# Kernel optimization log

Measured on AMD Instinct MI355X. Metric: run time of the kernel, lower is better.

The kernel has to match this reference:

```python
import jax, jax.numpy as jnp
import numpy as np

NUM_IMGS = 8192
NUM_CAPS = 8192
R = 7        # views per image
D = 256      # embedding dim


def setup_inputs() -> dict:
    key = jax.random.key(0)
    k1, k2 = jax.random.split(key)
    imgs = jax.random.normal(k1, (NUM_IMGS, R, D), dtype=jnp.float32)
    caps = jax.random.normal(k2, (NUM_CAPS, D), dtype=jnp.float32)
    return {"imgs": imgs, "caps": caps}


def reference(imgs, caps):
    # scores[i, r, c] = <imgs[i, r], caps[c]>  then max over views r
    # matches torch.matmul(imgs, caps.t()).max(1)[0]
    scores = jnp.einsum("ird,cd->irc", imgs, caps)  # [num_imgs, r, num_caps]
    return scores.max(axis=1)                        # [num_imgs, num_caps]
```

## Files before the change

kernel.cpp:

```cpp
#include <hip/hip_runtime.h>
#include <hip/hip_bf16.h>
#include <cstdint>
#include <cstddef>

#define NI 8192
#define NC 8192
#define RV 7
#define DD 256

typedef __bf16  bf16x8 __attribute__((ext_vector_type(8)));
typedef float   f32x4  __attribute__((ext_vector_type(4)));
typedef __fp16  f16x2  __attribute__((ext_vector_type(2)));

#define IMGS_WS_BYTES (32u * 56u * 16384u)
#define CAPS_WS_OFF   IMGS_WS_BYTES
#define CAPS_WS_BYTES (64u * 65536u)
#define WS_NEEDED     ((size_t)(IMGS_WS_BYTES + CAPS_WS_BYTES))

static __device__ __forceinline__ unsigned pkbf(float x, float y) {
  unsigned a = __float_as_uint(x) + 0x8000u;
  unsigned b = __float_as_uint(y) + 0x8000u;
  return __builtin_amdgcn_perm(b, a, 0x07060302u);
}

static __device__ __forceinline__ void gload16(const void* g, void* l) {
  __builtin_amdgcn_global_load_lds(
      (const __attribute__((address_space(1))) void*)g,
      (__attribute__((address_space(3))) void*)l, 16, 0, 0);
}

__global__ __launch_bounds__(256)
void conv_imgs(const float* __restrict__ imgs, uint4* __restrict__ ws) {
  unsigned T = blockIdx.x * 256u + threadIdx.x;
  unsigned img = T / 224u;
  unsigned rem = T - img * 224u;
  unsigned r  = rem >> 5;
  unsigned ju = rem & 31u;
  const float* s = imgs + ((size_t)img * RV + r) * DD + ju * 8u;
  float4 a = *(const float4*)s;
  float4 b = *(const float4*)(s + 4);
  uint4 v = { pkbf(a.x, a.y), pkbf(a.z, a.w), pkbf(b.x, b.y), pkbf(b.z, b.w) };
  unsigned ib = img >> 8, lrow = img & 255u;
  unsigned j = ju >> 2, u = ju & 3u;
  unsigned t = r * 8u + j;
  unsigned byteoff = (ib * 56u + t) * 16384u + u * 4096u + lrow * 16u;
  ws[byteoff >> 4] = v;
}

__global__ __launch_bounds__(256)
void conv_caps(const float* __restrict__ caps, uint4* __restrict__ ws) {
  unsigned T = blockIdx.x * 256u + threadIdx.x;
  unsigned gr = T >> 5;
  unsigned ju = T & 31u;
  const float* s = caps + (size_t)gr * DD + ju * 8u;
  float4 a = *(const float4*)s;
  float4 b = *(const float4*)(s + 4);
  uint4 v = { pkbf(a.x, a.y), pkbf(a.z, a.w), pkbf(b.x, b.y), pkbf(b.z, b.w) };
  unsigned cb = gr >> 7, row = gr & 127u;
  unsigned j = ju >> 2, u = ju & 3u;
  unsigned byteoff = cb * 65536u + j * 8192u + u * 2048u + row * 16u;
  ws[byteoff >> 4] = v;
}

#define LOAD_SET(P, BUFN, JN)                                   \
  P##a0 = *(const bf16x8*)(aF + (BUFN)*16384 + 0*256);          \
  P##a1 = *(const bf16x8*)(aF + (BUFN)*16384 + 1*256);          \
  P##a2 = *(const bf16x8*)(aF + (BUFN)*16384 + 2*256);          \
  P##a3 = *(const bf16x8*)(aF + (BUFN)*16384 + 3*256);          \
  P##b0 = *(const bf16x8*)(bF + (JN)*8192 + 0*256);             \
  P##b1 = *(const bf16x8*)(bF + (JN)*8192 + 1*256);             \
  P##b2 = *(const bf16x8*)(bF + (JN)*8192 + 2*256);             \
  P##b3 = *(const bf16x8*)(bF + (JN)*8192 + 3*256);

#define MFMA_SET(P)                                                              \
  acc[0][0] = __builtin_amdgcn_mfma_f32_16x16x32_bf16(P##a0, P##b0, acc[0][0], 0, 0, 0); \
  acc[1][0] = __builtin_amdgcn_mfma_f32_16x16x32_bf16(P##a1, P##b0, acc[1][0], 0, 0, 0); \
  acc[2][0] = __builtin_amdgcn_mfma_f32_16x16x32_bf16(P##a2, P##b0, acc[2][0], 0, 0, 0); \
  acc[3][0] = __builtin_amdgcn_mfma_f32_16x16x32_bf16(P##a3, P##b0, acc[3][0], 0, 0, 0); \
  acc[0][1] = __builtin_amdgcn_mfma_f32_16x16x32_bf16(P##a0, P##b1, acc[0][1], 0, 0, 0); \
  acc[1][1] = __builtin_amdgcn_mfma_f32_16x16x32_bf16(P##a1, P##b1, acc[1][1], 0, 0, 0); \
  acc[2][1] = __builtin_amdgcn_mfma_f32_16x16x32_bf16(P##a2, P##b1, acc[2][1], 0, 0, 0); \
  acc[3][1] = __builtin_amdgcn_mfma_f32_16x16x32_bf16(P##a3, P##b1, acc[3][1], 0, 0, 0); \
  acc[0][2] = __builtin_amdgcn_mfma_f32_16x16x32_bf16(P##a0, P##b2, acc[0][2], 0, 0, 0); \
  acc[1][2] = __builtin_amdgcn_mfma_f32_16x16x32_bf16(P##a1, P##b2, acc[1][2], 0, 0, 0); \
  acc[2][2] = __builtin_amdgcn_mfma_f32_16x16x32_bf16(P##a2, P##b2, acc[2][2], 0, 0, 0); \
  acc[3][2] = __builtin_amdgcn_mfma_f32_16x16x32_bf16(P##a3, P##b2, acc[3][2], 0, 0, 0); \
  acc[0][3] = __builtin_amdgcn_mfma_f32_16x16x32_bf16(P##a0, P##b3, acc[0][3], 0, 0, 0); \
  acc[1][3] = __builtin_amdgcn_mfma_f32_16x16x32_bf16(P##a1, P##b3, acc[1][3], 0, 0, 0); \
  acc[2][3] = __builtin_amdgcn_mfma_f32_16x16x32_bf16(P##a2, P##b3, acc[2][3], 0, 0, 0); \
  acc[3][3] = __builtin_amdgcn_mfma_f32_16x16x32_bf16(P##a3, P##b3, acc[3][3], 0, 0, 0);

#define CHUNK(CUR, NXT, BUFN, JN)                                        \
  LOAD_SET(NXT, BUFN, JN)                                                \
  gload16(stp,        ldsA + (((BUFN)+2)&3)*16384 + wid*1024);           \
  gload16(stp + 8192, ldsA + (((BUFN)+2)&3)*16384 + 8192 + wid*1024);    \
  stp += 16384;                                                          \
  __builtin_amdgcn_s_setprio(1);                                         \
  MFMA_SET(CUR)                                                          \
  __builtin_amdgcn_s_setprio(0);                                         \
  asm volatile("s_waitcnt vmcnt(2)" ::: "memory");                       \
  __builtin_amdgcn_s_barrier();                                          \
  asm volatile("" ::: "memory");

__global__ __launch_bounds__(512, 2)
void mvm_mfma(const char* __restrict__ wi, const char* __restrict__ wcap,
              float* __restrict__ out)
{
  __shared__ __align__(1024) char lds[131072];
  char* const ldsA = lds;
  char* const ldsB = lds + 65536;

  const int tid  = threadIdx.x;
  const int lane = tid & 63;
  const int wid  = tid >> 6;
  const int wm   = wid >> 1;
  const int wn   = wid & 1;

  const int bid = (int)blockIdx.x;
  const int swz = (bid & 7) * 256 + (bid >> 3);
  const int ib  = swz >> 6;
  const int cb  = swz & 63;

  const char* abase = wi   + (size_t)ib * (56u * 16384u);
  const char* bbase = wcap + (size_t)cb * 65536u;

  #pragma unroll
  for (int l = 0; l < 8; ++l)
    gload16(bbase + l * 8192 + tid * 16, ldsB + l * 8192 + wid * 1024);
  #pragma unroll
  for (int c = 0; c < 3; ++c) {
    gload16(abase + c * 16384 + tid * 16,        ldsA + c * 16384 + wid * 1024);
    gload16(abase + c * 16384 + 8192 + tid * 16, ldsA + c * 16384 + 8192 + wid * 1024);
  }
  asm volatile("s_waitcnt vmcnt(2)" ::: "memory");
  __builtin_amdgcn_s_barrier();
  asm volatile("" ::: "memory");

  const int lrow = lane & 15;
  const int lu   = lane >> 4;
  const char* const aF = ldsA + lu * 4096 + (wm * 64 + lrow) * 16;
  const char* const bF = ldsB + lu * 2048 + (wn * 64 + lrow) * 16;
  const char* stp = abase + 3 * 16384 + tid * 16;

  bf16x8 s0a0, s0a1, s0a2, s0a3, s0b0, s0b1, s0b2, s0b3;
  bf16x8 s1a0, s1a1, s1a2, s1a3, s1b0, s1b1, s1b2, s1b3;
  LOAD_SET(s0, 0, 0)

  f16x2 om[4][4][2];
  #pragma unroll
  for (int m = 0; m < 4; ++m)
    #pragma unroll
    for (int n = 0; n < 4; ++n)
      #pragma unroll
      for (int h = 0; h < 2; ++h)
        om[m][n][h] = (f16x2){(__fp16)-65504.f, (__fp16)-65504.f};

  f32x4 acc[4][4];

  #pragma unroll 1
  for (int r = 0; r < RV; ++r) {
    #pragma unroll
    for (int m = 0; m < 4; ++m)
      #pragma unroll
      for (int n = 0; n < 4; ++n)
        acc[m][n] = (f32x4){0.f, 0.f, 0.f, 0.f};

    CHUNK(s0, s1, 1, 1)
    CHUNK(s1, s0, 2, 2)
    CHUNK(s0, s1, 3, 3)
    CHUNK(s1, s0, 0, 4)
    CHUNK(s0, s1, 1, 5)
    CHUNK(s1, s0, 2, 6)
    CHUNK(s0, s1, 3, 7)
    CHUNK(s1, s0, 0, 0)

    #pragma unroll
    for (int m = 0; m < 4; ++m)
      #pragma unroll
      for (int n = 0; n < 4; ++n) {
        f16x2 lo = __builtin_amdgcn_cvt_pkrtz(acc[m][n][0], acc[m][n][1]);
        f16x2 hi = __builtin_amdgcn_cvt_pkrtz(acc[m][n][2], acc[m][n][3]);
        om[m][n][0] = __builtin_elementwise_max(om[m][n][0], lo);
        om[m][n][1] = __builtin_elementwise_max(om[m][n][1], hi);
      }
  }

  const int rbase = ib * 256 + wm * 64;
  const int cbase = cb * 128 + wn * 64;
  #pragma unroll
  for (int m = 0; m < 4; ++m)
    #pragma unroll
    for (int h = 0; h < 2; ++h)
      #pragma unroll
      for (int e = 0; e < 2; ++e) {
        size_t ro = (size_t)(rbase + m * 16 + lu * 4 + h * 2 + e) * NC + cbase + lrow;
        #pragma unroll
        for (int n = 0; n < 4; ++n)
          out[ro + n * 16] = (float)om[m][n][h][e];
      }
}

__global__ __launch_bounds__(512, 1)
void mvm_fallback(const float* __restrict__ imgs, const float* __restrict__ caps,
                  float* __restrict__ out)
{
  __shared__ __align__(16) char ldsB[128 * 512];
  __shared__ __align__(16) char ldsA[2][256 * 128];

  const int tid  = threadIdx.x;
  const int lane = tid & 63;
  const int wid  = tid >> 6;
  const int wr   = wid >> 1;
  const int wc   = wid & 1;
  const int i0   = blockIdx.y * 256;
  const int c0   = blockIdx.x * 128;

  #pragma unroll
  for (int it = 0; it < 8; ++it) {
    int c    = tid + it * 512;
    int row  = c >> 5;
    int colb = (c & 31) * 16;
    const float* p = caps + (size_t)(c0 + row) * DD + (c & 31) * 8;
    float4 a = *(const float4*)p;
    float4 b = *(const float4*)(p + 4);
    uint4 v;
    v.x = pkbf(a.x, a.y); v.y = pkbf(a.z, a.w);
    v.z = pkbf(b.x, b.y); v.w = pkbf(b.z, b.w);
    *(uint4*)(ldsB + row * 512 + (colb ^ ((row & 7) << 4))) = v;
  }
  #pragma unroll
  for (int it = 0; it < 4; ++it) {
    int c    = tid + it * 512;
    int row  = c >> 3;
    int colb = (c & 7) * 16;
    const float* p = imgs + ((size_t)(i0 + row) * RV + 0) * DD + (c & 7) * 8;
    float4 a = *(const float4*)p;
    float4 b = *(const float4*)(p + 4);
    uint4 v;
    v.x = pkbf(a.x, a.y); v.y = pkbf(a.z, a.w);
    v.z = pkbf(b.x, b.y); v.w = pkbf(b.z, b.w);
    *(uint4*)(ldsA[0] + row * 128 + (colb ^ ((row & 7) << 4))) = v;
  }
  __syncthreads();

  f32x4 omax[4][4];
  #pragma unroll
  for (int m = 0; m < 4; ++m)
    #pragma unroll
    for (int n = 0; n < 4; ++n)
      #pragma unroll
      for (int j = 0; j < 4; ++j)
        omax[m][n][j] = -3.4e38f;

  f32x4 acc[4][4];
  int cur = 0;
  const int lrow = lane & 15;
  const int lkb  = (lane >> 4) * 16;

  for (int ch = 0; ch < RV * 4; ++ch) {
    const int kc = ch & 3;
    if (kc == 0) {
      #pragma unroll
      for (int m = 0; m < 4; ++m)
        #pragma unroll
        for (int n = 0; n < 4; ++n)
          acc[m][n] = (f32x4){0.f, 0.f, 0.f, 0.f};
    }
    const int  chn  = ch + 1;
    const bool hasn = (chn < RV * 4);
    float4 pf[8];
    if (hasn) {
      const int rn = chn >> 2;
      const int kn = (chn & 3) * 64;
      #pragma unroll
      for (int it = 0; it < 4; ++it) {
        int c   = tid + it * 512;
        int row = c >> 3;
        const float* p = imgs + ((size_t)(i0 + row) * RV + rn) * DD + kn + (c & 7) * 8;
        pf[2 * it]     = *(const float4*)p;
        pf[2 * it + 1] = *(const float4*)(p + 4);
      }
    }
    #pragma unroll
    for (int ks = 0; ks < 2; ++ks) {
      bf16x8 af[4], bfr[4];
      #pragma unroll
      for (int m = 0; m < 4; ++m) {
        int row = wr * 64 + m * 16 + lrow;
        af[m] = *(const bf16x8*)(ldsA[cur] + row * 128 + ((ks * 64 + lkb) ^ ((row & 7) << 4)));
      }
      #pragma unroll
      for (int n = 0; n < 4; ++n) {
        int row = wc * 64 + n * 16 + lrow;
        bfr[n] = *(const bf16x8*)(ldsB + row * 512 + (((ch & 3) * 128 + ks * 64 + lkb) ^ ((row & 7) << 4)));
      }
      #pragma unroll
      for (int m = 0; m < 4; ++m)
        #pragma unroll
        for (int n = 0; n < 4; ++n)
          acc[m][n] = __builtin_amdgcn_mfma_f32_16x16x32_bf16(af[m], bfr[n], acc[m][n], 0, 0, 0);
    }
    if (hasn) {
      #pragma unroll
      for (int it = 0; it < 4; ++it) {
        int c    = tid + it * 512;
        int row  = c >> 3;
        int colb = (c & 7) * 16;
        uint4 v;
        v.x = pkbf(pf[2 * it].x,     pf[2 * it].y);
        v.y = pkbf(pf[2 * it].z,     pf[2 * it].w);
        v.z = pkbf(pf[2 * it + 1].x, pf[2 * it + 1].y);
        v.w = pkbf(pf[2 * it + 1].z, pf[2 * it + 1].w);
        *(uint4*)(ldsA[cur ^ 1] + row * 128 + (colb ^ ((row & 7) << 4))) = v;
      }
    }
    __syncthreads();
    cur ^= 1;
    if (kc == 3) {
      #pragma unroll
      for (int m = 0; m < 4; ++m)
        #pragma unroll
        for (int n = 0; n < 4; ++n)
          #pragma unroll
          for (int j = 0; j < 4; ++j)
            omax[m][n][j] = fmaxf(omax[m][n][j], acc[m][n][j]);
    }
  }

  const int rbase = i0 + wr * 64;
  const int cbase = c0 + wc * 64;
  const int lr4   = (lane >> 4) * 4;
  const int lc    = lane & 15;
  #pragma unroll
  for (int m = 0; m < 4; ++m)
    #pragma unroll
    for (int j = 0; j < 4; ++j) {
      size_t ro = (size_t)(rbase + m * 16 + lr4 + j) * NC;
      #pragma unroll
      for (int n = 0; n < 4; ++n)
        out[ro + cbase + n * 16 + lc] = omax[m][n][j];
    }
}

extern "C" void kernel_launch(void* const* d_in, const int* in_sizes, int n_in,
                              void* d_out, int out_size, void* d_ws, size_t ws_size,
                              hipStream_t stream) {
  const float* imgs = (const float*)d_in[0];
  const float* caps = (const float*)d_in[1];
  float* out = (float*)d_out;

  if (ws_size >= WS_NEEDED) {
    char* ws = (char*)d_ws;
    conv_imgs<<<7168, 256, 0, stream>>>(imgs, (uint4*)ws);
    conv_caps<<<1024, 256, 0, stream>>>(caps, (uint4*)(ws + CAPS_WS_OFF));
    mvm_mfma<<<2048, 512, 0, stream>>>((const char*)ws, (const char*)(ws + CAPS_WS_OFF), out);
  } else {
    dim3 grid(NC / 128, NI / 256);
    mvm_fallback<<<grid, 512, 0, stream>>>(imgs, caps, out);
  }
}
```

Baseline: 264.3 us.

## Shrink MFMA block tile to 128x128 with 4 waves and double-buffered A

Changes the main GEMM-max kernel from 256x128 tiles with 8 waves to 128x128 tiles with 4 waves. The image workspace layout is rebuilt to match, and the grid doubles to 4096 blocks. The A pipeline drops from a 4-slot ring with vmcnt(2) to a 2-slot double buffer that waits vmcnt(0) each chunk, which cuts LDS per block to 80KB. The aim is better occupancy and load balance across CUs, at the cost of more redundant caps loads per output, a shallower prefetch and stricter per-chunk syncs.

```diff
diff --git a/kernel.cpp b/kernel.cpp
--- a/kernel.cpp
+++ b/kernel.cpp
@@ -12,7 +12,7 @@
 typedef float   f32x4  __attribute__((ext_vector_type(4)));
 typedef __fp16  f16x2  __attribute__((ext_vector_type(2)));
 
-#define IMGS_WS_BYTES (32u * 56u * 16384u)
+#define IMGS_WS_BYTES (64u * 56u * 8192u)
 #define CAPS_WS_OFF   IMGS_WS_BYTES
 #define CAPS_WS_BYTES (64u * 65536u)
 #define WS_NEEDED     ((size_t)(IMGS_WS_BYTES + CAPS_WS_BYTES))
@@ -40,10 +40,10 @@
   float4 a = *(const float4*)s;
   float4 b = *(const float4*)(s + 4);
   uint4 v = { pkbf(a.x, a.y), pkbf(a.z, a.w), pkbf(b.x, b.y), pkbf(b.z, b.w) };
-  unsigned ib = img >> 8, lrow = img & 255u;
+  unsigned ib = img >> 7, lrow = img & 127u;
   unsigned j = ju >> 2, u = ju & 3u;
   unsigned t = r * 8u + j;
-  unsigned byteoff = (ib * 56u + t) * 16384u + u * 4096u + lrow * 16u;
+  unsigned byteoff = (ib * 56u + t) * 8192u + u * 2048u + lrow * 16u;
   ws[byteoff >> 4] = v;
 }
 
@@ -62,53 +62,56 @@
   ws[byteoff >> 4] = v;
 }
 
-#define LOAD_SET(P, BUFN, JN)                                   \
-  P##a0 = *(const bf16x8*)(aF + (BUFN)*16384 + 0*256);          \
-  P##a1 = *(const bf16x8*)(aF + (BUFN)*16384 + 1*256);          \
-  P##a2 = *(const bf16x8*)(aF + (BUFN)*16384 + 2*256);          \
-  P##a3 = *(const bf16x8*)(aF + (BUFN)*16384 + 3*256);          \
-  P##b0 = *(const bf16x8*)(bF + (JN)*8192 + 0*256);             \
-  P##b1 = *(const bf16x8*)(bF + (JN)*8192 + 1*256);             \
-  P##b2 = *(const bf16x8*)(bF + (JN)*8192 + 2*256);             \
-  P##b3 = *(const bf16x8*)(bF + (JN)*8192 + 3*256);
-
-#define MFMA_SET(P)                                                              \
-  acc[0][0] = __builtin_amdgcn_mfma_f32_16x16x32_bf16(P##a0, P##b0, acc[0][0], 0, 0, 0); \
-  acc[1][0] = __builtin_amdgcn_mfma_f32_16x16x32_bf16(P##a1, P##b0, acc[1][0], 0, 0, 0); \
-  acc[2][0] = __builtin_amdgcn_mfma_f32_16x16x32_bf16(P##a2, P##b0, acc[2][0], 0, 0, 0); \
-  acc[3][0] = __builtin_amdgcn_mfma_f32_16x16x32_bf16(P##a3, P##b0, acc[3][0], 0, 0, 0); \
-  acc[0][1] = __builtin_amdgcn_mfma_f32_16x16x32_bf16(P##a0, P##b1, acc[0][1], 0, 0, 0); \
-  acc[1][1] = __builtin_amdgcn_mfma_f32_16x16x32_bf16(P##a1, P##b1, acc[1][1], 0, 0, 0); \
-  acc[2][1] = __builtin_amdgcn_mfma_f32_16x16x32_bf16(P##a2, P##b1, acc[2][1], 0, 0, 0); \
-  acc[3][1] = __builtin_amdgcn_mfma_f32_16x16x32_bf16(P##a3, P##b1, acc[3][1], 0, 0, 0); \
-  acc[0][2] = __builtin_amdgcn_mfma_f32_16x16x32_bf16(P##a0, P##b2, acc[0][2], 0, 0, 0); \
-  acc[1][2] = __builtin_amdgcn_mfma_f32_16x16x32_bf16(P##a1, P##b2, acc[1][2], 0, 0, 0); \
-  acc[2][2] = __builtin_amdgcn_mfma_f32_16x16x32_bf16(P##a2, P##b2, acc[2][2], 0, 0, 0); \
-  acc[3][2] = __builtin_amdgcn_mfma_f32_16x16x32_bf16(P##a3, P##b2, acc[3][2], 0, 0, 0); \
-  acc[0][3] = __builtin_amdgcn_mfma_f32_16x16x32_bf16(P##a0, P##b3, acc[0][3], 0, 0, 0); \
-  acc[1][3] = __builtin_amdgcn_mfma_f32_16x16x32_bf16(P##a1, P##b3, acc[1][3], 0, 0, 0); \
-  acc[2][3] = __builtin_amdgcn_mfma_f32_16x16x32_bf16(P##a2, P##b3, acc[2][3], 0, 0, 0); \
-  acc[3][3] = __builtin_amdgcn_mfma_f32_16x16x32_bf16(P##a3, P##b3, acc[3][3], 0, 0, 0);
-
-#define CHUNK(CUR, NXT, BUFN, JN)                                        \
-  LOAD_SET(NXT, BUFN, JN)                                                \
-  gload16(stp,        ldsA + (((BUFN)+2)&3)*16384 + wid*1024);           \
-  gload16(stp + 8192, ldsA + (((BUFN)+2)&3)*16384 + 8192 + wid*1024);    \
-  stp += 16384;                                                          \
-  __builtin_amdgcn_s_setprio(1);                                         \
-  MFMA_SET(CUR)                                                          \
-  __builtin_amdgcn_s_setprio(0);                                         \
-  asm volatile("s_waitcnt vmcnt(2)" ::: "memory");                       \
-  __builtin_amdgcn_s_barrier();                                          \
-  asm volatile("" ::: "memory");
-
-__global__ __launch_bounds__(512, 2)
+#define BLOAD(P, JN)                                            \
+  P##0 = *(const bf16x8*)(bF + (JN)*8192 + 0*256);              \
+  P##1 = *(const bf16x8*)(bF + (JN)*8192 + 1*256);              \
+  P##2 = *(const bf16x8*)(bF + (JN)*8192 + 2*256);              \
+  P##3 = *(const bf16x8*)(bF + (JN)*8192 + 3*256);
+
+#define CHUNK(BP, BN, PBUF, JNXT, MORE)                                  \
+  {                                                                      \
+    bf16x8 a0 = *(const bf16x8*)(aF + (PBUF)*8192 + 0*256);              \
+    bf16x8 a1 = *(const bf16x8*)(aF + (PBUF)*8192 + 1*256);              \
+    bf16x8 a2 = *(const bf16x8*)(aF + (PBUF)*8192 + 2*256);              \
+    bf16x8 a3 = *(const bf16x8*)(aF + (PBUF)*8192 + 3*256);              \
+    BLOAD(BN, JNXT)                                                      \
+    if (MORE) {                                                          \
+      gload16(stp,        ldsA + ((PBUF)^1)*8192 + wid*1024);            \
+      gload16(stp + 4096, ldsA + ((PBUF)^1)*8192 + 4096 + wid*1024);     \
+      stp += 8192;                                                       \
+    }                                                                    \
+    __builtin_amdgcn_s_setprio(1);                                       \
+    acc[0][0] = __builtin_amdgcn_mfma_f32_16x16x32_bf16(a0, BP##0, acc[0][0], 0, 0, 0); \
+    acc[1][0] = __builtin_amdgcn_mfma_f32_16x16x32_bf16(a1, BP##0, acc[1][0], 0, 0, 0); \
+    acc[2][0] = __builtin_amdgcn_mfma_f32_16x16x32_bf16(a2, BP##0, acc[2][0], 0, 0, 0); \
+    acc[3][0] = __builtin_amdgcn_mfma_f32_16x16x32_bf16(a3, BP##0, acc[3][0], 0, 0, 0); \
+    acc[0][1] = __builtin_amdgcn_mfma_f32_16x16x32_bf16(a0, BP##1, acc[0][1], 0, 0, 0); \
+    acc[1][1] = __builtin_amdgcn_mfma_f32_16x16x32_bf16(a1, BP##1, acc[1][1], 0, 0, 0); \
+    acc[2][1] = __builtin_amdgcn_mfma_f32_16x16x32_bf16(a2, BP##1, acc[2][1], 0, 0, 0); \
+    acc[3][1] = __builtin_amdgcn_mfma_f32_16x16x32_bf16(a3, BP##1, acc[3][1], 0, 0, 0); \
+    acc[0][2] = __builtin_amdgcn_mfma_f32_16x16x32_bf16(a0, BP##2, acc[0][2], 0, 0, 0); \
+    acc[1][2] = __builtin_amdgcn_mfma_f32_16x16x32_bf16(a1, BP##2, acc[1][2], 0, 0, 0); \
+    acc[2][2] = __builtin_amdgcn_mfma_f32_16x16x32_bf16(a2, BP##2, acc[2][2], 0, 0, 0); \
+    acc[3][2] = __builtin_amdgcn_mfma_f32_16x16x32_bf16(a3, BP##2, acc[3][2], 0, 0, 0); \
+    acc[0][3] = __builtin_amdgcn_mfma_f32_16x16x32_bf16(a0, BP##3, acc[0][3], 0, 0, 0); \
+    acc[1][3] = __builtin_amdgcn_mfma_f32_16x16x32_bf16(a1, BP##3, acc[1][3], 0, 0, 0); \
+    acc[2][3] = __builtin_amdgcn_mfma_f32_16x16x32_bf16(a2, BP##3, acc[2][3], 0, 0, 0); \
+    acc[3][3] = __builtin_amdgcn_mfma_f32_16x16x32_bf16(a3, BP##3, acc[3][3], 0, 0, 0); \
+    __builtin_amdgcn_s_setprio(0);                                       \
+    if (MORE) {                                                          \
+      asm volatile("s_waitcnt vmcnt(0)" ::: "memory");                   \
+      __builtin_amdgcn_s_barrier();                                      \
+      asm volatile("" ::: "memory");                                     \
+    }                                                                    \
+  }
+
+__global__ __launch_bounds__(256, 2)
 void mvm_mfma(const char* __restrict__ wi, const char* __restrict__ wcap,
               float* __restrict__ out)
 {
-  __shared__ __align__(1024) char lds[131072];
-  char* const ldsA = lds;
-  char* const ldsB = lds + 65536;
+  __shared__ __align__(1024) char lds[81920];
+  char* const ldsB = lds;
+  char* const ldsA = lds + 65536;
 
   const int tid  = threadIdx.x;
   const int lane = tid & 63;
@@ -117,34 +120,30 @@
   const int wn   = wid & 1;
 
   const int bid = (int)blockIdx.x;
-  const int swz = (bid & 7) * 256 + (bid >> 3);
+  const int swz = (bid & 7) * 512 + (bid >> 3);
   const int ib  = swz >> 6;
   const int cb  = swz & 63;
 
-  const char* abase = wi   + (size_t)ib * (56u * 16384u);
+  const char* abase = wi   + (size_t)ib * (56u * 8192u);
   const char* bbase = wcap + (size_t)cb * 65536u;
 
   #pragma unroll
-  for (int l = 0; l < 8; ++l)
-    gload16(bbase + l * 8192 + tid * 16, ldsB + l * 8192 + wid * 1024);
-  #pragma unroll
-  for (int c = 0; c < 3; ++c) {
-    gload16(abase + c * 16384 + tid * 16,        ldsA + c * 16384 + wid * 1024);
-    gload16(abase + c * 16384 + 8192 + tid * 16, ldsA + c * 16384 + 8192 + wid * 1024);
-  }
-  asm volatile("s_waitcnt vmcnt(2)" ::: "memory");
+  for (int l = 0; l < 16; ++l)
+    gload16(bbase + l * 4096 + tid * 16, ldsB + l * 4096 + wid * 1024);
+  gload16(abase + tid * 16,        ldsA + wid * 1024);
+  gload16(abase + 4096 + tid * 16, ldsA + 4096 + wid * 1024);
+  asm volatile("s_waitcnt vmcnt(0)" ::: "memory");
   __builtin_amdgcn_s_barrier();
   asm volatile("" ::: "memory");
 
   const int lrow = lane & 15;
   const int lu   = lane >> 4;
-  const char* const aF = ldsA + lu * 4096 + (wm * 64 + lrow) * 16;
+  const char* const aF = ldsA + lu * 2048 + (wm * 64 + lrow) * 16;
   const char* const bF = ldsB + lu * 2048 + (wn * 64 + lrow) * 16;
-  const char* stp = abase + 3 * 16384 + tid * 16;
-
-  bf16x8 s0a0, s0a1, s0a2, s0a3, s0b0, s0b1, s0b2, s0b3;
-  bf16x8 s1a0, s1a1, s1a2, s1a3, s1b0, s1b1, s1b2, s1b3;
-  LOAD_SET(s0, 0, 0)
+  const char* stp = abase + 8192 + tid * 16;
+
+  bf16x8 bc0, bc1, bc2, bc3, bn0, bn1, bn2, bn3;
+  BLOAD(bc, 0)
 
   f16x2 om[4][4][2];
   #pragma unroll
@@ -159,20 +158,21 @@
 
   #pragma unroll 1
   for (int r = 0; r < RV; ++r) {
+    const bool lastr = (r == RV - 1);
     #pragma unroll
     for (int m = 0; m < 4; ++m)
       #pragma unroll
       for (int n = 0; n < 4; ++n)
         acc[m][n] = (f32x4){0.f, 0.f, 0.f, 0.f};
 
-    CHUNK(s0, s1, 1, 1)
-    CHUNK(s1, s0, 2, 2)
-    CHUNK(s0, s1, 3, 3)
-    CHUNK(s1, s0, 0, 4)
-    CHUNK(s0, s1, 1, 5)
-    CHUNK(s1, s0, 2, 6)
-    CHUNK(s0, s1, 3, 7)
-    CHUNK(s1, s0, 0, 0)
+    CHUNK(bc, bn, 0, 1, true)
+    CHUNK(bn, bc, 1, 2, true)
+    CHUNK(bc, bn, 0, 3, true)
+    CHUNK(bn, bc, 1, 4, true)
+    CHUNK(bc, bn, 0, 5, true)
+    CHUNK(bn, bc, 1, 6, true)
+    CHUNK(bc, bn, 0, 7, true)
+    CHUNK(bn, bc, 1, 0, !lastr)
 
     #pragma unroll
     for (int m = 0; m < 4; ++m)
@@ -185,7 +185,7 @@
       }
   }
 
-  const int rbase = ib * 256 + wm * 64;
+  const int rbase = ib * 128 + wm * 64;
   const int cbase = cb * 128 + wn * 64;
   #pragma unroll
   for (int m = 0; m < 4; ++m)
@@ -353,7 +353,7 @@
     char* ws = (char*)d_ws;
     conv_imgs<<<7168, 256, 0, stream>>>(imgs, (uint4*)ws);
     conv_caps<<<1024, 256, 0, stream>>>(caps, (uint4*)(ws + CAPS_WS_OFF));
-    mvm_mfma<<<2048, 512, 0, stream>>>((const char*)ws, (const char*)(ws + CAPS_WS_OFF), out);
+    mvm_mfma<<<4096, 256, 0, stream>>>((const char*)ws, (const char*)(ws + CAPS_WS_OFF), out);
   } else {
     dim3 grid(NC / 128, NI / 256);
     mvm_fallback<<<grid, 512, 0, stream>>>(imgs, caps, out);
```

After: 276.6 us. 4.6% more time.

## Load image operand directly from global into registers, dropping LDS staging

Applied to the files above, without the earlier changes.

Stops staging image fragments through a four-slot LDS ring and instead has each wave load its A fragments from global memory straight into registers, one chunk ahead of the MFMAs. This removes the per-chunk async LDS copies, the vmcnt waits and the barriers, and halves the LDS footprint to just the caption tile, which may let two blocks share a CU. In exchange, global-memory latency is hidden only by one chunk of MFMAs plus occupancy. Waves sharing rows now issue duplicate global loads, and the final prefetch reads past the block's slice of the buffer.

```diff
diff --git a/kernel.cpp b/kernel.cpp
--- a/kernel.cpp
+++ b/kernel.cpp
@@ -62,53 +62,42 @@
   ws[byteoff >> 4] = v;
 }
 
-#define LOAD_SET(P, BUFN, JN)                                   \
-  P##a0 = *(const bf16x8*)(aF + (BUFN)*16384 + 0*256);          \
-  P##a1 = *(const bf16x8*)(aF + (BUFN)*16384 + 1*256);          \
-  P##a2 = *(const bf16x8*)(aF + (BUFN)*16384 + 2*256);          \
-  P##a3 = *(const bf16x8*)(aF + (BUFN)*16384 + 3*256);          \
-  P##b0 = *(const bf16x8*)(bF + (JN)*8192 + 0*256);             \
-  P##b1 = *(const bf16x8*)(bF + (JN)*8192 + 1*256);             \
-  P##b2 = *(const bf16x8*)(bF + (JN)*8192 + 2*256);             \
-  P##b3 = *(const bf16x8*)(bF + (JN)*8192 + 3*256);
-
-#define MFMA_SET(P)                                                              \
-  acc[0][0] = __builtin_amdgcn_mfma_f32_16x16x32_bf16(P##a0, P##b0, acc[0][0], 0, 0, 0); \
-  acc[1][0] = __builtin_amdgcn_mfma_f32_16x16x32_bf16(P##a1, P##b0, acc[1][0], 0, 0, 0); \
-  acc[2][0] = __builtin_amdgcn_mfma_f32_16x16x32_bf16(P##a2, P##b0, acc[2][0], 0, 0, 0); \
-  acc[3][0] = __builtin_amdgcn_mfma_f32_16x16x32_bf16(P##a3, P##b0, acc[3][0], 0, 0, 0); \
-  acc[0][1] = __builtin_amdgcn_mfma_f32_16x16x32_bf16(P##a0, P##b1, acc[0][1], 0, 0, 0); \
-  acc[1][1] = __builtin_amdgcn_mfma_f32_16x16x32_bf16(P##a1, P##b1, acc[1][1], 0, 0, 0); \
-  acc[2][1] = __builtin_amdgcn_mfma_f32_16x16x32_bf16(P##a2, P##b1, acc[2][1], 0, 0, 0); \
-  acc[3][1] = __builtin_amdgcn_mfma_f32_16x16x32_bf16(P##a3, P##b1, acc[3][1], 0, 0, 0); \
-  acc[0][2] = __builtin_amdgcn_mfma_f32_16x16x32_bf16(P##a0, P##b2, acc[0][2], 0, 0, 0); \
-  acc[1][2] = __builtin_amdgcn_mfma_f32_16x16x32_bf16(P##a1, P##b2, acc[1][2], 0, 0, 0); \
-  acc[2][2] = __builtin_amdgcn_mfma_f32_16x16x32_bf16(P##a2, P##b2, acc[2][2], 0, 0, 0); \
-  acc[3][2] = __builtin_amdgcn_mfma_f32_16x16x32_bf16(P##a3, P##b2, acc[3][2], 0, 0, 0); \
-  acc[0][3] = __builtin_amdgcn_mfma_f32_16x16x32_bf16(P##a0, P##b3, acc[0][3], 0, 0, 0); \
-  acc[1][3] = __builtin_amdgcn_mfma_f32_16x16x32_bf16(P##a1, P##b3, acc[1][3], 0, 0, 0); \
-  acc[2][3] = __builtin_amdgcn_mfma_f32_16x16x32_bf16(P##a2, P##b3, acc[2][3], 0, 0, 0); \
-  acc[3][3] = __builtin_amdgcn_mfma_f32_16x16x32_bf16(P##a3, P##b3, acc[3][3], 0, 0, 0);
-
-#define CHUNK(CUR, NXT, BUFN, JN)                                        \
-  LOAD_SET(NXT, BUFN, JN)                                                \
-  gload16(stp,        ldsA + (((BUFN)+2)&3)*16384 + wid*1024);           \
-  gload16(stp + 8192, ldsA + (((BUFN)+2)&3)*16384 + 8192 + wid*1024);    \
-  stp += 16384;                                                          \
-  __builtin_amdgcn_s_setprio(1);                                         \
-  MFMA_SET(CUR)                                                          \
-  __builtin_amdgcn_s_setprio(0);                                         \
-  asm volatile("s_waitcnt vmcnt(2)" ::: "memory");                       \
-  __builtin_amdgcn_s_barrier();                                          \
-  asm volatile("" ::: "memory");
+#define CHUNK(AC, AN, BC, BN, JNXT)                                      \
+  {                                                                      \
+    AN##0 = *(const bf16x8*)(ap + 0 * 256);                              \
+    AN##1 = *(const bf16x8*)(ap + 1 * 256);                              \
+    AN##2 = *(const bf16x8*)(ap + 2 * 256);                              \
+    AN##3 = *(const bf16x8*)(ap + 3 * 256);                              \
+    BN##0 = *(const bf16x8*)(bF + (JNXT) * 8192 + 0 * 256);              \
+    BN##1 = *(const bf16x8*)(bF + (JNXT) * 8192 + 1 * 256);              \
+    BN##2 = *(const bf16x8*)(bF + (JNXT) * 8192 + 2 * 256);              \
+    BN##3 = *(const bf16x8*)(bF + (JNXT) * 8192 + 3 * 256);              \
+    ap += 16384;                                                         \
+    __builtin_amdgcn_s_setprio(1);                                       \
+    acc[0][0] = __builtin_amdgcn_mfma_f32_16x16x32_bf16(AC##0, BC##0, acc[0][0], 0, 0, 0); \
+    acc[1][0] = __builtin_amdgcn_mfma_f32_16x16x32_bf16(AC##1, BC##0, acc[1][0], 0, 0, 0); \
+    acc[2][0] = __builtin_amdgcn_mfma_f32_16x16x32_bf16(AC##2, BC##0, acc[2][0], 0, 0, 0); \
+    acc[3][0] = __builtin_amdgcn_mfma_f32_16x16x32_bf16(AC##3, BC##0, acc[3][0], 0, 0, 0); \
+    acc[0][1] = __builtin_amdgcn_mfma_f32_16x16x32_bf16(AC##0, BC##1, acc[0][1], 0, 0, 0); \
+    acc[1][1] = __builtin_amdgcn_mfma_f32_16x16x32_bf16(AC##1, BC##1, acc[1][1], 0, 0, 0); \
+    acc[2][1] = __builtin_amdgcn_mfma_f32_16x16x32_bf16(AC##2, BC##1, acc[2][1], 0, 0, 0); \
+    acc[3][1] = __builtin_amdgcn_mfma_f32_16x16x32_bf16(AC##3, BC##1, acc[3][1], 0, 0, 0); \
+    acc[0][2] = __builtin_amdgcn_mfma_f32_16x16x32_bf16(AC##0, BC##2, acc[0][2], 0, 0, 0); \
+    acc[1][2] = __builtin_amdgcn_mfma_f32_16x16x32_bf16(AC##1, BC##2, acc[1][2], 0, 0, 0); \
+    acc[2][2] = __builtin_amdgcn_mfma_f32_16x16x32_bf16(AC##2, BC##2, acc[2][2], 0, 0, 0); \
+    acc[3][2] = __builtin_amdgcn_mfma_f32_16x16x32_bf16(AC##3, BC##2, acc[3][2], 0, 0, 0); \
+    acc[0][3] = __builtin_amdgcn_mfma_f32_16x16x32_bf16(AC##0, BC##3, acc[0][3], 0, 0, 0); \
+    acc[1][3] = __builtin_amdgcn_mfma_f32_16x16x32_bf16(AC##1, BC##3, acc[1][3], 0, 0, 0); \
+    acc[2][3] = __builtin_amdgcn_mfma_f32_16x16x32_bf16(AC##2, BC##3, acc[2][3], 0, 0, 0); \
+    acc[3][3] = __builtin_amdgcn_mfma_f32_16x16x32_bf16(AC##3, BC##3, acc[3][3], 0, 0, 0); \
+    __builtin_amdgcn_s_setprio(0);                                       \
+  }
 
 __global__ __launch_bounds__(512, 2)
 void mvm_mfma(const char* __restrict__ wi, const char* __restrict__ wcap,
               float* __restrict__ out)
 {
-  __shared__ __align__(1024) char lds[131072];
-  char* const ldsA = lds;
-  char* const ldsB = lds + 65536;
+  __shared__ __align__(1024) char ldsB[65536];
 
   const int tid  = threadIdx.x;
   const int lane = tid & 63;
@@ -127,24 +116,27 @@
   #pragma unroll
   for (int l = 0; l < 8; ++l)
     gload16(bbase + l * 8192 + tid * 16, ldsB + l * 8192 + wid * 1024);
-  #pragma unroll
-  for (int c = 0; c < 3; ++c) {
-    gload16(abase + c * 16384 + tid * 16,        ldsA + c * 16384 + wid * 1024);
-    gload16(abase + c * 16384 + 8192 + tid * 16, ldsA + c * 16384 + 8192 + wid * 1024);
-  }
-  asm volatile("s_waitcnt vmcnt(2)" ::: "memory");
+  asm volatile("s_waitcnt vmcnt(0)" ::: "memory");
   __builtin_amdgcn_s_barrier();
   asm volatile("" ::: "memory");
 
   const int lrow = lane & 15;
   const int lu   = lane >> 4;
-  const char* const aF = ldsA + lu * 4096 + (wm * 64 + lrow) * 16;
+  const char* ap = abase + lu * 4096 + (wm * 64 + lrow) * 16;
   const char* const bF = ldsB + lu * 2048 + (wn * 64 + lrow) * 16;
-  const char* stp = abase + 3 * 16384 + tid * 16;
-
-  bf16x8 s0a0, s0a1, s0a2, s0a3, s0b0, s0b1, s0b2, s0b3;
-  bf16x8 s1a0, s1a1, s1a2, s1a3, s1b0, s1b1, s1b2, s1b3;
-  LOAD_SET(s0, 0, 0)
+
+  bf16x8 Ac0, Ac1, Ac2, Ac3, An0, An1, An2, An3;
+  bf16x8 Bc0, Bc1, Bc2, Bc3, Bn0, Bn1, Bn2, Bn3;
+
+  Ac0 = *(const bf16x8*)(ap + 0 * 256);
+  Ac1 = *(const bf16x8*)(ap + 1 * 256);
+  Ac2 = *(const bf16x8*)(ap + 2 * 256);
+  Ac3 = *(const bf16x8*)(ap + 3 * 256);
+  Bc0 = *(const bf16x8*)(bF + 0 * 256);
+  Bc1 = *(const bf16x8*)(bF + 1 * 256);
+  Bc2 = *(const bf16x8*)(bF + 2 * 256);
+  Bc3 = *(const bf16x8*)(bF + 3 * 256);
+  ap += 16384;
 
   f16x2 om[4][4][2];
   #pragma unroll
@@ -165,14 +157,14 @@
       for (int n = 0; n < 4; ++n)
         acc[m][n] = (f32x4){0.f, 0.f, 0.f, 0.f};
 
-    CHUNK(s0, s1, 1, 1)
-    CHUNK(s1, s0, 2, 2)
-    CHUNK(s0, s1, 3, 3)
-    CHUNK(s1, s0, 0, 4)
-    CHUNK(s0, s1, 1, 5)
-    CHUNK(s1, s0, 2, 6)
-    CHUNK(s0, s1, 3, 7)
-    CHUNK(s1, s0, 0, 0)
+    CHUNK(Ac, An, Bc, Bn, 1)
+    CHUNK(An, Ac, Bn, Bc, 2)
+    CHUNK(Ac, An, Bc, Bn, 3)
+    CHUNK(An, Ac, Bn, Bc, 4)
+    CHUNK(Ac, An, Bc, Bn, 5)
+    CHUNK(An, Ac, Bn, Bc, 6)
+    CHUNK(Ac, An, Bc, Bn, 7)
+    CHUNK(An, Ac, Bn, Bc, 0)
 
     #pragma unroll
     for (int m = 0; m < 4; ++m)
```

Measured after the change: 271.8 us. 1.03x slower.
